# Performance work log

Hardware: AMD Instinct MI355X
Metric: run time of the kernel (lower is better)

## Reference

```python
import jax, jax.numpy as jnp
import numpy as np

GATE_DECAY = 3.0

def setup_inputs() -> dict:
    key = jax.random.key(0)
    ks = jax.random.split(key, 4)
    B, S, D, I = 8, 2048, 512, 2048
    x = jax.random.normal(ks[0], (B, S, D), dtype=jnp.float32)
    # kaiming normal fan_in, linear gain: std = 1/sqrt(fan_in)
    Wa = jax.random.normal(ks[1], (I, D), dtype=jnp.float32) / np.sqrt(D)
    Wi = jax.random.normal(ks[2], (I, D), dtype=jnp.float32) / np.sqrt(D)
    ba = jnp.zeros((I,), dtype=jnp.float32)
    bi = jnp.zeros((I,), dtype=jnp.float32)
    lo, hi = np.log(0.9 / 0.1), np.log(0.999 / 0.001)  # logit(0.9), logit(0.999)
    gate = jax.random.uniform(ks[3], (I,), dtype=jnp.float32, minval=lo, maxval=hi)
    return {"x": x, "Wa": Wa, "ba": ba, "Wi": Wi, "bi": bi, "gate": gate}

def reference(x, Wa, ba, Wi, bi, gate):
    # Precompute both projections for all timesteps as large GEMMs.
    pa = jnp.einsum('bsd,id->bsi', x, Wa) + ba   # [B,S,I]
    pi = jnp.einsum('bsd,id->bsi', x, Wi) + bi   # [B,S,I]
    reset_gate = jax.nn.sigmoid(pa)
    input_gate = jax.nn.sigmoid(pi)
    alpha = jax.nn.sigmoid(gate)                  # [I]
    adaptive_alpha = alpha / (GATE_DECAY ** reset_gate)          # [B,S,I]
    drive = jnp.sqrt(1.0 - adaptive_alpha ** 2) * (input_gate * pi)
    B, S, I = pa.shape

    def step(h, ac):
        a, c = ac
        h = a * h + c
        return h, h

    h0 = jnp.zeros((B, I), dtype=x.dtype)
    # scan over time: move S to leading axis
    _, ys = jax.lax.scan(step, h0, (adaptive_alpha.transpose(1, 0, 2), drive.transpose(1, 0, 2)))
    return ys.transpose(1, 0, 2)  # [B,S,I]
```

## Files before the change

kernel.cpp:

```cpp
#include <hip/hip_runtime.h>


#define LOG2_3 1.5849625007211562f

typedef _Float16 f16x8 __attribute__((ext_vector_type(8)));
typedef _Float16 f16x4 __attribute__((ext_vector_type(4)));
typedef _Float16 f16x2 __attribute__((ext_vector_type(2)));
typedef float f32x4 __attribute__((ext_vector_type(4)));

__device__ __forceinline__ float sigmoidf_(float v) {
  return 1.0f / (1.0f + __expf(-v));
}

__device__ __forceinline__ void async_copy16(void* lds, const void* gp) {
  __builtin_amdgcn_global_load_lds((__attribute__((address_space(1))) void*)gp,
                                   (__attribute__((address_space(3))) void*)lds,
                                   16, 0, 0);
}

__global__ __launch_bounds__(256) void cvt_all(const float* __restrict__ x,
                                               const float* __restrict__ Wa,
                                               const float* __restrict__ Wi,
                                               _Float16* __restrict__ xh,
                                               _Float16* __restrict__ wh) {
  int idx = blockIdx.x * 256 + threadIdx.x;
  const float* src;
  _Float16* dst;
  int off, doff;
  if (idx < 2097152) {
    src = x; dst = xh; off = idx; doff = idx;
  } else if (idx < 2097152 + 262144) {
    src = Wa; dst = wh; off = idx - 2097152;
    doff = off + ((off >> 7) << 7);
  } else {
    src = Wi; dst = wh; off = idx - 2359296;
    doff = off + ((off >> 7) << 7) + 128;
  }
  float4 v = ((const float4*)src)[off];
  f16x4 h;
  h[0] = (_Float16)v.x;
  h[1] = (_Float16)v.y;
  h[2] = (_Float16)v.z;
  h[3] = (_Float16)v.w;
  ((f16x4*)dst)[doff] = h;
}

__device__ __forceinline__ void gate_ac(float pa, float pi, float alpha, float& a, float& c) {
  float rg = sigmoidf_(pa);
  a = alpha * exp2f(-LOG2_3 * rg);
  float ig = sigmoidf_(pi);
  c = sqrtf(fmaxf(1.0f - a * a, 0.0f)) * (ig * pi);
}

__global__ __launch_bounds__(256) void gemm_gate(const _Float16* __restrict__ Ah,
                                                 const _Float16* __restrict__ Wh,
                                                 const float* __restrict__ ba,
                                                 const float* __restrict__ bi,
                                                 const float* __restrict__ gate,
                                                 _Float16* __restrict__ AC,
                                                 float2* __restrict__ agg) {
  constexpr int K = 512;
  constexpr int N2 = 4096;
  __shared__ __align__(16) _Float16 smem[16384];
  __shared__ float pAs[8 * 65];
  __shared__ float pHs[8 * 65];
  const int t = threadIdx.x;
  const int mBase = blockIdx.y * 128;
  const int nBase = blockIdx.x * 128;
  const int r = t >> 2;
  const int p = t & 3;
  const int lsw = p ^ ((r >> 1) & 3);
  const _Float16* gA0 = Ah + (size_t)(mBase + r) * K + lsw * 8;
  const _Float16* gB0 = Wh + (size_t)(nBase + r) * K + lsw * 8;
  const int ldst = r * 32 + p * 8;

  const int lane = t & 63;
  const int wave = t >> 6;
  const int wm = (wave & 1) * 64;
  const int wn = (wave >> 1) * 64;
  const int lrow = lane & 15;
  const int quad = lane >> 4;
  const int xq = quad ^ ((lrow >> 1) & 3);

  f32x4 acc[4][4];
#pragma unroll
  for (int i = 0; i < 4; ++i)
#pragma unroll
    for (int j = 0; j < 4; ++j)
      acc[i][j] = (f32x4)0.0f;

  _Float16* b0 = smem;
  _Float16* b1 = smem + 8192;

  async_copy16(b0 + ldst, gA0);
  async_copy16(b0 + 2048 + ldst, gA0 + (size_t)64 * K);
  async_copy16(b0 + 4096 + ldst, gB0);
  async_copy16(b0 + 6144 + ldst, gB0 + (size_t)64 * K);
  __syncthreads();

#pragma unroll
  for (int kt = 0; kt < 16; ++kt) {
    _Float16* cur = (kt & 1) ? b1 : b0;
    _Float16* nxt = (kt & 1) ? b0 : b1;
    if (kt < 15) {
      const int ko = (kt + 1) * 32;
      async_copy16(nxt + ldst, gA0 + ko);
      async_copy16(nxt + 2048 + ldst, gA0 + (size_t)64 * K + ko);
      async_copy16(nxt + 4096 + ldst, gB0 + ko);
      async_copy16(nxt + 6144 + ldst, gB0 + (size_t)64 * K + ko);
    }
    f16x8 af[4], bf[4];
#pragma unroll
    for (int i = 0; i < 4; ++i)
      af[i] = *(const f16x8*)(cur + (wm + i * 16 + lrow) * 32 + xq * 8);
#pragma unroll
    for (int j = 0; j < 4; ++j)
      bf[j] = *(const f16x8*)(cur + 4096 + (wn + j * 16 + lrow) * 32 + xq * 8);
#pragma unroll
    for (int i = 0; i < 4; ++i)
#pragma unroll
      for (int j = 0; j < 4; ++j)
        acc[i][j] = __builtin_amdgcn_mfma_f32_16x16x32_f16(af[i], bf[j], acc[i][j], 0, 0, 0);
    __syncthreads();
  }

  float bias[4];
#pragma unroll
  for (int j = 0; j < 4; ++j) {
    const int n = nBase + wn + j * 16 + lrow;
    bias[j] = (n & 1) ? bi[n >> 1] : ba[n >> 1];
  }

  const int col = t & 63;
  const int q = t >> 6;
  const float alpha = sigmoidf_(gate[(nBase >> 1) + col]);
  const int b = blockIdx.y >> 4;

#pragma unroll
  for (int h = 0; h < 2; ++h) {
    if (wm == h * 64) {
#pragma unroll
      for (int i = 0; i < 4; ++i)
#pragma unroll
        for (int j = 0; j < 4; ++j)
#pragma unroll
          for (int rr = 0; rr < 4; ++rr)
            smem[(i * 16 + quad * 4 + rr) * 136 + wn + j * 16 + lrow] =
                (_Float16)(acc[i][j][rr] + bias[j]);
    }
    __syncthreads();
    float A = 1.0f, Hn = 0.0f;
    _Float16* ACp = AC + (size_t)(mBase + h * 64 + q * 16) * N2 + nBase + 2 * col;
#pragma unroll 4
    for (int rs = 0; rs < 16; ++rs) {
      f16x2 pp = *(const f16x2*)(smem + (q * 16 + rs) * 136 + 2 * col);
      float a, c;
      gate_ac((float)pp[0], (float)pp[1], alpha, a, c);
      f16x2 o;
      o[0] = (_Float16)a;
      o[1] = (_Float16)c;
      *(f16x2*)ACp = o;
      ACp += N2;
      A *= a;
      Hn = fmaf(a, Hn, c);
    }
    pAs[(h * 4 + q) * 65 + col] = A;
    pHs[(h * 4 + q) * 65 + col] = Hn;
    __syncthreads();
  }

  if (t < 64) {
#pragma unroll
    for (int k = 0; k < 4; ++k) {
      float A0 = pAs[(2 * k) * 65 + t], H0 = pHs[(2 * k) * 65 + t];
      float A1 = pAs[(2 * k + 1) * 65 + t], H1 = pHs[(2 * k + 1) * 65 + t];
      const int ch = ((blockIdx.y & 15) << 2) + k;
      agg[((size_t)(b * 64 + ch)) * 2048 + (nBase >> 1) + t] =
          make_float2(A0 * A1, fmaf(A1, H0, H1));
    }
  }
}

__global__ __launch_bounds__(64) void scan_pass2(const float2* __restrict__ agg,
                                                 float* __restrict__ carry) {
  const int i = blockIdx.x * 64 + threadIdx.x;
  const int b = blockIdx.y;
  float h = 0.0f;
  for (int c8 = 0; c8 < 8; ++c8) {
    float2 aH[8];
#pragma unroll
    for (int u = 0; u < 8; ++u)
      aH[u] = agg[((size_t)(b * 64 + c8 * 8 + u)) * 2048 + i];
#pragma unroll
    for (int u = 0; u < 8; ++u) {
      carry[((size_t)(b * 64 + c8 * 8 + u)) * 2048 + i] = h;
      h = fmaf(aH[u].x, h, aH[u].y);
    }
  }
}

__global__ __launch_bounds__(256) void scan_out(const _Float16* __restrict__ AC,
                                                const float* __restrict__ carry,
                                                float* __restrict__ out) {
  const int tt = blockIdx.x * 256 + threadIdx.x;
  const int i0 = tt * 4;
  const int ch = blockIdx.y;
  const int b = blockIdx.z;
  const float4 cr = ((const float4*)(carry + ((size_t)(b * 64 + ch)) * 2048))[tt];
  float h0 = cr.x, h1 = cr.y, h2 = cr.z, h3 = cr.w;
  const _Float16* row = AC + ((size_t)(b * 2048 + ch * 32)) * 4096 + i0 * 2;
  float* orow = out + ((size_t)(b * 2048 + ch * 32)) * 2048 + i0;
  for (int s4 = 0; s4 < 8; ++s4) {
    f16x8 v[4];
#pragma unroll
    for (int u = 0; u < 4; ++u)
      v[u] = *(const f16x8*)(row + (size_t)u * 4096);
    row += 4 * 4096;
#pragma unroll
    for (int u = 0; u < 4; ++u) {
      h0 = fmaf((float)v[u][0], h0, (float)v[u][1]);
      h1 = fmaf((float)v[u][2], h1, (float)v[u][3]);
      h2 = fmaf((float)v[u][4], h2, (float)v[u][5]);
      h3 = fmaf((float)v[u][6], h3, (float)v[u][7]);
      float4 o;
      o.x = h0;
      o.y = h1;
      o.z = h2;
      o.w = h3;
      *(float4*)(orow + (size_t)u * 2048) = o;
    }
    orow += 4 * 2048;
  }
}

extern "C" void kernel_launch(void* const* d_in, const int* in_sizes, int n_in,
                              void* d_out, int out_size, void* d_ws, size_t ws_size,
                              hipStream_t stream) {
  const float* x = (const float*)d_in[0];
  const float* Wa = (const float*)d_in[1];
  const float* ba = (const float*)d_in[2];
  const float* Wi = (const float*)d_in[3];
  const float* bi = (const float*)d_in[4];
  const float* gate = (const float*)d_in[5];
  float* out = (float*)d_out;

  char* ws = (char*)d_ws;
  _Float16* xh = (_Float16*)ws;
  _Float16* wh = (_Float16*)(ws + 16777216);
  const size_t MN2 = (size_t)16384 * 4096;
  _Float16* AC = (_Float16*)(ws + 20971520);
  float2* agg = (float2*)(ws + 20971520 + MN2 * 2);
  float* carry = (float*)(ws + 20971520 + MN2 * 2 + 8388608);

  cvt_all<<<10240, 256, 0, stream>>>(x, Wa, Wi, xh, wh);
  gemm_gate<<<dim3(32, 128), 256, 0, stream>>>(xh, wh, ba, bi, gate, AC, agg);
  scan_pass2<<<dim3(32, 8), 64, 0, stream>>>(agg, carry);
  scan_out<<<dim3(2, 64, 8), 256, 0, stream>>>(AC, carry, out);
}
```

Baseline: 344.1 us.

## Triple-buffer GEMM K-loop with prefetch distance two and manual vmcnt waits

Replaces the double-buffered async global-to-LDS pipeline in the fused GEMM+gate kernel with a three-stage ring buffer that prefetches two K-tiles ahead. Explicit s_waitcnt vmcnt(4) and a single raw s_barrier per iteration replace the end-of-loop __syncthreads, so loads for tile kt+1 can stay in flight while tile kt is computed. This is meant to hide more global load latency. In exchange, LDS use grows from 32KB to 48KB per block, which may lower occupancy, and correctness depends on the hand-written waitcnt accounting.

```diff
diff --git a/kernel.cpp b/kernel.cpp
--- a/kernel.cpp
+++ b/kernel.cpp
@@ -61,7 +61,7 @@
                                                  float2* __restrict__ agg) {
   constexpr int K = 512;
   constexpr int N2 = 4096;
-  __shared__ __align__(16) _Float16 smem[16384];
+  __shared__ __align__(16) _Float16 smem[24576];
   __shared__ float pAs[8 * 65];
   __shared__ float pHs[8 * 65];
   const int t = threadIdx.x;
@@ -89,26 +89,29 @@
     for (int j = 0; j < 4; ++j)
       acc[i][j] = (f32x4)0.0f;
 
-  _Float16* b0 = smem;
-  _Float16* b1 = smem + 8192;
-
-  async_copy16(b0 + ldst, gA0);
-  async_copy16(b0 + 2048 + ldst, gA0 + (size_t)64 * K);
-  async_copy16(b0 + 4096 + ldst, gB0);
-  async_copy16(b0 + 6144 + ldst, gB0 + (size_t)64 * K);
-  __syncthreads();
+  auto STAGE = [&](int tt) {
+    _Float16* bb = smem + 8192 * (tt % 3);
+    const int ko = tt * 32;
+    async_copy16(bb + ldst, gA0 + ko);
+    async_copy16(bb + 2048 + ldst, gA0 + (size_t)64 * K + ko);
+    async_copy16(bb + 4096 + ldst, gB0 + ko);
+    async_copy16(bb + 6144 + ldst, gB0 + (size_t)64 * K + ko);
+  };
+
+  STAGE(0);
+  STAGE(1);
 
 #pragma unroll
   for (int kt = 0; kt < 16; ++kt) {
-    _Float16* cur = (kt & 1) ? b1 : b0;
-    _Float16* nxt = (kt & 1) ? b0 : b1;
-    if (kt < 15) {
-      const int ko = (kt + 1) * 32;
-      async_copy16(nxt + ldst, gA0 + ko);
-      async_copy16(nxt + 2048 + ldst, gA0 + (size_t)64 * K + ko);
-      async_copy16(nxt + 4096 + ldst, gB0 + ko);
-      async_copy16(nxt + 6144 + ldst, gB0 + (size_t)64 * K + ko);
-    }
+    if (kt == 15)
+      asm volatile("s_waitcnt vmcnt(0) lgkmcnt(0)" ::: "memory");
+    else
+      asm volatile("s_waitcnt vmcnt(4) lgkmcnt(0)" ::: "memory");
+    __builtin_amdgcn_sched_barrier(0);
+    __builtin_amdgcn_s_barrier();
+    __builtin_amdgcn_sched_barrier(0);
+    if (kt < 14) STAGE(kt + 2);
+    const _Float16* cur = smem + 8192 * (kt % 3);
     f16x8 af[4], bf[4];
 #pragma unroll
     for (int i = 0; i < 4; ++i)
@@ -121,8 +124,8 @@
 #pragma unroll
       for (int j = 0; j < 4; ++j)
         acc[i][j] = __builtin_amdgcn_mfma_f32_16x16x32_f16(af[i], bf[j], acc[i][j], 0, 0, 0);
-    __syncthreads();
-  }
+  }
+  __syncthreads();
 
   float bias[4];
 #pragma unroll
```

Result: no change. 339.0 us (-1.5%).
